# Kernel optimization log

Hardware: AMD Instinct MI355X
Metric: run time of the kernel (lower is better)

## Reference

```python
import jax, jax.numpy as jnp
import numpy as np

N_NODES = 50000
N_EDGES = 800000
D = 128
# PNA avg_deg['log'] from deg histogram: all 50000 nodes have degree 16
# avg_deg_log = sum(log(i+1)*deg[i]) / sum(deg) = log(17)
AVG_DEG_LOG = float(np.log(17.0))
EPS = 1e-5  # PyG StdAggregation epsilon


def setup_inputs() -> dict:
    key = jax.random.key(0)
    k1, k2, k3 = jax.random.split(key, 3)
    x = jax.random.normal(k1, (N_EDGES, D), jnp.float32)
    index = jax.random.randint(k2, (N_EDGES,), 0, N_NODES)
    # nn.Linear(12*D, D): weight [out, in]
    W = jax.random.normal(k3, (D, 12 * D), jnp.float32) * 0.02
    b = jnp.zeros((D,), jnp.float32)
    return {"x": x, "index": index, "W": W, "b": b}


def reference(x, index, W, b):
    N = N_NODES
    ones = jnp.ones((x.shape[0],), x.dtype)
    cnt = jax.ops.segment_sum(ones, index, num_segments=N)          # [N] degree
    cnt_c = jnp.maximum(cnt, 1.0)[:, None]                          # clamp(1)
    s1 = jax.ops.segment_sum(x, index, num_segments=N)              # [N, D]
    s2 = jax.ops.segment_sum(x * x, index, num_segments=N)          # [N, D]
    mean = s1 / cnt_c
    var = s2 / cnt_c - mean * mean
    std = jnp.sqrt(jax.nn.relu(var) + EPS)
    mn = jax.ops.segment_min(x, index, num_segments=N)
    mx = jax.ops.segment_max(x, index, num_segments=N)
    empty = (cnt == 0.0)[:, None]
    mn = jnp.where(empty, 0.0, mn)  # torch_scatter fills empty segments with 0
    mx = jnp.where(empty, 0.0, mx)
    agg = jnp.concatenate([mean, mn, mx, std], axis=-1)             # [N, 4D]
    logd = jnp.log(jnp.maximum(cnt, 1.0) + 1.0)[:, None]
    amp = agg * (logd / AVG_DEG_LOG)                                # amplification
    att = agg * (AVG_DEG_LOG / logd)                                # attenuation
    out = jnp.concatenate([agg, amp, att], axis=-1)                 # [N, 12D]
    return out @ W.T + b                                            # [N, D]
```

## Files before the change

kernel.cpp:

```cpp
#include <hip/hip_runtime.h>
#include <hip/hip_bf16.h>

typedef __attribute__((ext_vector_type(8))) __bf16 bf16x8;
typedef __attribute__((ext_vector_type(4))) float f32x4;

#define AVG_DEG_LOG 2.833213344056216f

__device__ __forceinline__ unsigned short f2bf(float f) {
  union { float f; unsigned int u; } a; a.f = f;
  unsigned int r = a.u + 0x7FFFu + ((a.u >> 16) & 1u);
  return (unsigned short)(r >> 16);
}

__device__ __forceinline__ uint2 pack4(f32x4 a) {
  uint2 u;
  u.x = (unsigned)f2bf(a[0]) | ((unsigned)f2bf(a[1]) << 16);
  u.y = (unsigned)f2bf(a[2]) | ((unsigned)f2bf(a[3]) << 16);
  return u;
}

__global__ void hist_wconv_kernel(const int* __restrict__ idx, int* __restrict__ cnt, int E,
                                  int hb, const float* __restrict__ W,
                                  unsigned short* __restrict__ Wb, int n4) {
  int b = blockIdx.x;
  if (b < hb) {
    int i = b * 256 + threadIdx.x;
    if (i < E) atomicAdd(&cnt[idx[i]], 1);
  } else {
    int i = (b - hb) * 256 + threadIdx.x;
    if (i < n4) {
      float4 v = ((const float4*)W)[i];
      ushort4 o;
      o.x = f2bf(v.x); o.y = f2bf(v.y); o.z = f2bf(v.z); o.w = f2bf(v.w);
      ((ushort4*)Wb)[i] = o;
    }
  }
}

__global__ __launch_bounds__(1024) void scan_kernel(const int* __restrict__ cnt,
                                                    int* __restrict__ offsets, int N) {
  __shared__ int partial[1024];
  int t = threadIdx.x;
  int CH = (N + 1023) >> 10;
  int base = t * CH;
  int s = 0;
  for (int i = 0; i < CH; ++i) { int id = base + i; if (id < N) s += cnt[id]; }
  partial[t] = s;
  __syncthreads();
  int val = s;
  for (int off = 1; off < 1024; off <<= 1) {
    int add = (t >= off) ? partial[t - off] : 0;
    __syncthreads();
    val += add;
    partial[t] = val;
    __syncthreads();
  }
  int run = val - s;
  for (int i = 0; i < CH; ++i) {
    int id = base + i;
    if (id < N) { offsets[id] = run; run += cnt[id]; }
  }
  if (t == 1023) offsets[N] = run;
}

__global__ void scatter_kernel(const int* __restrict__ idx, const int* __restrict__ offsets,
                               int* __restrict__ cursor, int* __restrict__ edge_ids, int E) {
  int i = blockIdx.x * blockDim.x + threadIdx.x;
  if (i < E) {
    int n = idx[i];
    int p = atomicAdd(&cursor[n], 1);
    edge_ids[offsets[n] + p] = i;
  }
}

__global__ __launch_bounds__(256) void agg_kernel(const float* __restrict__ x,
    const int* __restrict__ edge_ids, const int* __restrict__ offsets,
    unsigned short* __restrict__ agg4, float* __restrict__ amp, float* __restrict__ att, int Nn) {
  int wid = blockIdx.x * 4 + (threadIdx.x >> 6);
  if (wid >= Nn) return;
  int lane = threadIdx.x & 63;
  int half = lane >> 5;
  int fh = (lane & 31) * 4;
  int offs = offsets[wid];
  int deg = offsets[wid + 1] - offs;
  f32x4 s = {0.f, 0.f, 0.f, 0.f}, q = {0.f, 0.f, 0.f, 0.f};
  f32x4 mn = {INFINITY, INFINITY, INFINITY, INFINITY};
  f32x4 mx = {-INFINITY, -INFINITY, -INFINITY, -INFINITY};
  const float* xb = x + fh;
  for (int i = 0; i < deg; i += 64) {
    int myid = 0;
    if (i + lane < deg) myid = edge_ids[offs + i + lane];
    int c = deg - i; if (c > 64) c = 64;
    for (int ii = 0; ii < c; ii += 16) {
      int e[8];
      bool val[8];
#pragma unroll
      for (int k = 0; k < 8; ++k) {
        int p = ii + 2 * k + half;
        val[k] = p < c;
        int pc = val[k] ? p : c - 1;
        e[k] = __shfl(myid, pc, 64);
      }
      f32x4 v[8];
#pragma unroll
      for (int k = 0; k < 8; ++k)
        v[k] = __builtin_nontemporal_load((const f32x4*)(xb + (size_t)e[k] * 128));
#pragma unroll
      for (int k = 0; k < 8; ++k) {
#pragma unroll
        for (int j = 0; j < 4; ++j) {
          float f = v[k][j];
          float fs = val[k] ? f : 0.f;
          s[j] += fs;
          q[j] += f * fs;
          mn[j] = fminf(mn[j], val[k] ? f : INFINITY);
          mx[j] = fmaxf(mx[j], val[k] ? f : -INFINITY);
        }
      }
    }
  }
#pragma unroll
  for (int j = 0; j < 4; ++j) {
    s[j] += __shfl_xor(s[j], 32, 64);
    q[j] += __shfl_xor(q[j], 32, 64);
    mn[j] = fminf(mn[j], __shfl_xor(mn[j], 32, 64));
    mx[j] = fmaxf(mx[j], __shfl_xor(mx[j], 32, 64));
  }
  float cdeg = deg > 0 ? (float)deg : 1.0f;
  float inv = 1.0f / cdeg;
  f32x4 mean, sd;
#pragma unroll
  for (int j = 0; j < 4; ++j) {
    mean[j] = s[j] * inv;
    float var = q[j] * inv - mean[j] * mean[j];
    var = var > 0.f ? var : 0.f;
    sd[j] = sqrtf(var + 1e-5f);
  }
  if (deg == 0) {
#pragma unroll
    for (int j = 0; j < 4; ++j) { mn[j] = 0.f; mx[j] = 0.f; }
  }
  size_t rb = (size_t)wid * 512;
  if (half == 0) {
    *(uint2*)(agg4 + rb + fh)       = pack4(mean);
    *(uint2*)(agg4 + rb + 128 + fh) = pack4(mn);
  } else {
    *(uint2*)(agg4 + rb + 256 + fh) = pack4(mx);
    *(uint2*)(agg4 + rb + 384 + fh) = pack4(sd);
  }
  if (lane == 0) {
    float ld = logf(cdeg + 1.0f);
    amp[wid] = ld / AVG_DEG_LOG;
    att[wid] = AVG_DEG_LOG / ld;
  }
}

__global__ __launch_bounds__(256) void gemm_kernel(
    const unsigned short* __restrict__ agg4, const unsigned short* __restrict__ Wb,
    const float* __restrict__ amp, const float* __restrict__ att,
    const float* __restrict__ bias, float* __restrict__ out, int Nn) {
  __shared__ __align__(16) unsigned short As[64][40];
  __shared__ __align__(16) unsigned short Bs[3][128][40];
  __shared__ float ampS[64], attS[64];
  int t = threadIdx.x;
  int m0 = blockIdx.x * 64;
  if (t < 64) {
    int n = m0 + t; if (n > Nn - 1) n = Nn - 1;
    ampS[t] = amp[n]; attS[t] = att[n];
  }
  int wave = t >> 6, lane = t & 63;
  int arow = lane & 15, quad = lane >> 4;
  f32x4 acc[3][8];
#pragma unroll
  for (int g = 0; g < 3; ++g)
#pragma unroll
    for (int c8 = 0; c8 < 8; ++c8) acc[g][c8] = (f32x4){0.f, 0.f, 0.f, 0.f};

  int ar = t >> 2;
  int akc = (t & 3) * 8;
  int agr = m0 + ar; if (agr > Nn - 1) agr = Nn - 1;
  const unsigned short* aptr = agg4 + (size_t)agr * 512 + akc;

  for (int kk = 0; kk < 512; kk += 32) {
    __syncthreads();
    *(uint4*)&As[ar][akc] = *(const uint4*)(aptr + kk);
#pragma unroll
    for (int j = 0; j < 6; ++j) {
      int idx = t + j * 256;
      int g = idx >> 9;
      int rem = idx & 511;
      int n = rem >> 2;
      int kc = (rem & 3) * 8;
      *(uint4*)&Bs[g][n][kc] = *(const uint4*)(Wb + (size_t)n * 1536 + g * 512 + kk + kc);
    }
    __syncthreads();
    bf16x8 af = *(bf16x8*)&As[wave * 16 + arow][quad * 8];
#pragma unroll
    for (int g = 0; g < 3; ++g) {
#pragma unroll
      for (int c8 = 0; c8 < 8; ++c8) {
        bf16x8 bf = *(bf16x8*)&Bs[g][c8 * 16 + arow][quad * 8];
        acc[g][c8] = __builtin_amdgcn_mfma_f32_16x16x32_bf16(af, bf, acc[g][c8], 0, 0, 0);
      }
    }
  }
#pragma unroll
  for (int c8 = 0; c8 < 8; ++c8) {
    int col = c8 * 16 + arow;
    float bv = bias[col];
#pragma unroll
    for (int r = 0; r < 4; ++r) {
      int lrow = wave * 16 + quad * 4 + r;
      int n = m0 + lrow;
      if (n < Nn) {
        float o = acc[0][c8][r] + ampS[lrow] * acc[1][c8][r] + attS[lrow] * acc[2][c8][r] + bv;
        out[(size_t)n * 128 + col] = o;
      }
    }
  }
}

extern "C" void kernel_launch(void* const* d_in, const int* in_sizes, int n_in,
                              void* d_out, int out_size, void* d_ws, size_t ws_size,
                              hipStream_t stream) {
  const float* x     = (const float*)d_in[0];
  const int*   index = (const int*)d_in[1];
  const float* W     = (const float*)d_in[2];
  const float* bias  = (const float*)d_in[3];
  int E  = in_sizes[1];
  int Nn = out_size / 128;
  float* out = (float*)d_out;

  char* ws = (char*)d_ws;
  size_t off = 0;
  int* cnt     = (int*)(ws + off); off += (size_t)Nn * 4;
  int* cursor  = (int*)(ws + off); off += (size_t)Nn * 4;
  int* offsets = (int*)(ws + off); off += (size_t)(Nn + 1) * 4;
  off = (off + 255) & ~(size_t)255;
  int* edge_ids = (int*)(ws + off); off += (size_t)E * 4;
  off = (off + 255) & ~(size_t)255;
  unsigned short* agg4 = (unsigned short*)(ws + off); off += (size_t)Nn * 512 * 2;
  float* amp = (float*)(ws + off); off += (size_t)Nn * 4;
  float* att = (float*)(ws + off); off += (size_t)Nn * 4;
  off = (off + 255) & ~(size_t)255;
  unsigned short* Wb = (unsigned short*)(ws + off); off += (size_t)128 * 1536 * 2;

  hipMemsetAsync(ws, 0, (size_t)Nn * 8, stream);

  int eb = (E + 255) / 256;
  int n4 = 128 * 1536 / 4;
  int wb = (n4 + 255) / 256;
  hist_wconv_kernel<<<eb + wb, 256, 0, stream>>>(index, cnt, E, eb, W, Wb, n4);
  scan_kernel<<<1, 1024, 0, stream>>>(cnt, offsets, Nn);
  scatter_kernel<<<eb, 256, 0, stream>>>(index, offsets, cursor, edge_ids, E);
  agg_kernel<<<(Nn + 3) / 4, 256, 0, stream>>>(x, edge_ids, offsets, agg4, amp, att, Nn);
  gemm_kernel<<<(Nn + 63) / 64, 256, 0, stream>>>(agg4, Wb, amp, att, bias, out, Nn);
}
```

Baseline: 755.1 us.

## Parallelize offset scan across blocks and aggregate two nodes per wave

```diff
diff --git a/kernel.cpp b/kernel.cpp
--- a/kernel.cpp
+++ b/kernel.cpp
@@ -37,30 +37,57 @@
   }
 }
 
-__global__ __launch_bounds__(1024) void scan_kernel(const int* __restrict__ cnt,
-                                                    int* __restrict__ offsets, int N) {
-  __shared__ int partial[1024];
+__global__ __launch_bounds__(256) void scan1_kernel(const int* __restrict__ cnt,
+                                                    int* __restrict__ bsums, int N) {
+  __shared__ int red[256];
   int t = threadIdx.x;
-  int CH = (N + 1023) >> 10;
-  int base = t * CH;
-  int s = 0;
-  for (int i = 0; i < CH; ++i) { int id = base + i; if (id < N) s += cnt[id]; }
-  partial[t] = s;
+  int i = blockIdx.x * 256 + t;
+  int v = (i < N) ? cnt[i] : 0;
+  red[t] = v;
   __syncthreads();
-  int val = s;
-  for (int off = 1; off < 1024; off <<= 1) {
-    int add = (t >= off) ? partial[t - off] : 0;
+  for (int o = 128; o > 0; o >>= 1) {
+    if (t < o) red[t] += red[t + o];
+    __syncthreads();
+  }
+  if (t == 0) bsums[blockIdx.x] = red[0];
+}
+
+__global__ __launch_bounds__(256) void scan2_kernel(int* __restrict__ bsums, int nb) {
+  __shared__ int sS[256];
+  int t = threadIdx.x;
+  int v = (t < nb) ? bsums[t] : 0;
+  sS[t] = v;
+  __syncthreads();
+  int val = v;
+  for (int o = 1; o < 256; o <<= 1) {
+    int add = (t >= o) ? sS[t - o] : 0;
     __syncthreads();
     val += add;
-    partial[t] = val;
-    __syncthreads();
-  }
-  int run = val - s;
-  for (int i = 0; i < CH; ++i) {
-    int id = base + i;
-    if (id < N) { offsets[id] = run; run += cnt[id]; }
-  }
-  if (t == 1023) offsets[N] = run;
+    sS[t] = val;
+    __syncthreads();
+  }
+  if (t < nb) bsums[t] = val - v;
+}
+
+__global__ __launch_bounds__(256) void scan3_kernel(const int* __restrict__ cnt,
+                                                    const int* __restrict__ bsums,
+                                                    int* __restrict__ offsets, int N, int E) {
+  __shared__ int sS[256];
+  int t = threadIdx.x;
+  int i = blockIdx.x * 256 + t;
+  int v = (i < N) ? cnt[i] : 0;
+  sS[t] = v;
+  __syncthreads();
+  int val = v;
+  for (int o = 1; o < 256; o <<= 1) {
+    int add = (t >= o) ? sS[t - o] : 0;
+    __syncthreads();
+    val += add;
+    sS[t] = val;
+    __syncthreads();
+  }
+  if (i < N) offsets[i] = bsums[blockIdx.x] + val - v;
+  if (blockIdx.x == 0 && t == 0) offsets[N] = E;
 }
 
 __global__ void scatter_kernel(const int* __restrict__ idx, const int* __restrict__ offsets,
@@ -73,52 +100,49 @@
   }
 }
 
-__global__ __launch_bounds__(256) void agg_kernel(const float* __restrict__ x,
-    const int* __restrict__ edge_ids, const int* __restrict__ offsets,
-    unsigned short* __restrict__ agg4, float* __restrict__ amp, float* __restrict__ att, int Nn) {
-  int wid = blockIdx.x * 4 + (threadIdx.x >> 6);
-  if (wid >= Nn) return;
-  int lane = threadIdx.x & 63;
-  int half = lane >> 5;
-  int fh = (lane & 31) * 4;
-  int offs = offsets[wid];
-  int deg = offsets[wid + 1] - offs;
-  f32x4 s = {0.f, 0.f, 0.f, 0.f}, q = {0.f, 0.f, 0.f, 0.f};
-  f32x4 mn = {INFINITY, INFINITY, INFINITY, INFINITY};
-  f32x4 mx = {-INFINITY, -INFINITY, -INFINITY, -INFINITY};
-  const float* xb = x + fh;
+__device__ __forceinline__ void agg_accum_chunk(const float* __restrict__ xb, int eid,
+    int ii, int deg, int half, f32x4& s, f32x4& q, f32x4& mn, f32x4& mx) {
+  int e[8];
+  bool val[8];
+#pragma unroll
+  for (int k = 0; k < 8; ++k) {
+    int p = ii + 2 * k + half;
+    val[k] = p < deg;
+    int pc = val[k] ? p : deg - 1;
+    e[k] = __shfl(eid, pc, 64);
+  }
+  f32x4 v[8];
+#pragma unroll
+  for (int k = 0; k < 8; ++k)
+    v[k] = __builtin_nontemporal_load((const f32x4*)(xb + (size_t)e[k] * 128));
+#pragma unroll
+  for (int k = 0; k < 8; ++k) {
+#pragma unroll
+    for (int j = 0; j < 4; ++j) {
+      float f = v[k][j];
+      float fs = val[k] ? f : 0.f;
+      s[j] += fs;
+      q[j] += f * fs;
+      mn[j] = fminf(mn[j], val[k] ? f : INFINITY);
+      mx[j] = fmaxf(mx[j], val[k] ? f : -INFINITY);
+    }
+  }
+}
+
+__device__ void agg_one(const float* __restrict__ xb, const int* __restrict__ edge_ids,
+    int offs, int deg, int lane, int half, f32x4& s, f32x4& q, f32x4& mn, f32x4& mx) {
   for (int i = 0; i < deg; i += 64) {
     int myid = 0;
     if (i + lane < deg) myid = edge_ids[offs + i + lane];
     int c = deg - i; if (c > 64) c = 64;
-    for (int ii = 0; ii < c; ii += 16) {
-      int e[8];
-      bool val[8];
-#pragma unroll
-      for (int k = 0; k < 8; ++k) {
-        int p = ii + 2 * k + half;
-        val[k] = p < c;
-        int pc = val[k] ? p : c - 1;
-        e[k] = __shfl(myid, pc, 64);
-      }
-      f32x4 v[8];
-#pragma unroll
-      for (int k = 0; k < 8; ++k)
-        v[k] = __builtin_nontemporal_load((const f32x4*)(xb + (size_t)e[k] * 128));
-#pragma unroll
-      for (int k = 0; k < 8; ++k) {
-#pragma unroll
-        for (int j = 0; j < 4; ++j) {
-          float f = v[k][j];
-          float fs = val[k] ? f : 0.f;
-          s[j] += fs;
-          q[j] += f * fs;
-          mn[j] = fminf(mn[j], val[k] ? f : INFINITY);
-          mx[j] = fmaxf(mx[j], val[k] ? f : -INFINITY);
-        }
-      }
-    }
-  }
+    for (int ii = 0; ii < c; ii += 16)
+      agg_accum_chunk(xb, myid, ii, c, half, s, q, mn, mx);
+  }
+}
+
+__device__ void agg_finish(unsigned short* __restrict__ agg4, float* __restrict__ amp,
+    float* __restrict__ att, int wid, int deg, int lane, int half, int fh,
+    f32x4 s, f32x4 q, f32x4 mn, f32x4 mx) {
 #pragma unroll
   for (int j = 0; j < 4; ++j) {
     s[j] += __shfl_xor(s[j], 32, 64);
@@ -153,6 +177,100 @@
     amp[wid] = ld / AVG_DEG_LOG;
     att[wid] = AVG_DEG_LOG / ld;
   }
+}
+
+__global__ __launch_bounds__(256) void agg_kernel(const float* __restrict__ x,
+    const int* __restrict__ edge_ids, const int* __restrict__ offsets,
+    unsigned short* __restrict__ agg4, float* __restrict__ amp, float* __restrict__ att, int Nn) {
+  int gw = blockIdx.x * 4 + (threadIdx.x >> 6);
+  int nA = gw * 2, nB = nA + 1;
+  if (nA >= Nn) return;
+  bool hasB = nB < Nn;
+  int lane = threadIdx.x & 63;
+  int half = lane >> 5;
+  int fh = (lane & 31) * 4;
+  const float* xb = x + fh;
+
+  int o0 = offsets[nA];
+  int o1 = offsets[nA + 1];
+  int o2 = hasB ? offsets[nB + 1] : o1;
+  int offsA = o0, degA = o1 - o0;
+  int offsB = o1, degB = hasB ? (o2 - o1) : 0;
+
+  f32x4 sA = {0,0,0,0}, qA = {0,0,0,0};
+  f32x4 mnA = {INFINITY,INFINITY,INFINITY,INFINITY}, mxA = {-INFINITY,-INFINITY,-INFINITY,-INFINITY};
+  f32x4 sB = {0,0,0,0}, qB = {0,0,0,0};
+  f32x4 mnB = {INFINITY,INFINITY,INFINITY,INFINITY}, mxB = {-INFINITY,-INFINITY,-INFINITY,-INFINITY};
+
+  if (degA <= 64 && degB <= 64) {
+    int eidA = 0, eidB = 0;
+    if (lane < degA) eidA = edge_ids[offsA + lane];
+    if (lane < degB) eidB = edge_ids[offsB + lane];
+    int cm = degA > degB ? degA : degB;
+    for (int ii = 0; ii < cm; ii += 16) {
+      bool doA = ii < degA;
+      bool doB = ii < degB;
+      int eA[8], eB[8];
+      bool valA[8], valB[8];
+      f32x4 vA[8], vB[8];
+      if (doA) {
+#pragma unroll
+        for (int k = 0; k < 8; ++k) {
+          int p = ii + 2 * k + half;
+          valA[k] = p < degA;
+          int pc = valA[k] ? p : degA - 1;
+          eA[k] = __shfl(eidA, pc, 64);
+        }
+#pragma unroll
+        for (int k = 0; k < 8; ++k)
+          vA[k] = __builtin_nontemporal_load((const f32x4*)(xb + (size_t)eA[k] * 128));
+      }
+      if (doB) {
+#pragma unroll
+        for (int k = 0; k < 8; ++k) {
+          int p = ii + 2 * k + half;
+          valB[k] = p < degB;
+          int pc = valB[k] ? p : degB - 1;
+          eB[k] = __shfl(eidB, pc, 64);
+        }
+#pragma unroll
+        for (int k = 0; k < 8; ++k)
+          vB[k] = __builtin_nontemporal_load((const f32x4*)(xb + (size_t)eB[k] * 128));
+      }
+      if (doA) {
+#pragma unroll
+        for (int k = 0; k < 8; ++k) {
+#pragma unroll
+          for (int j = 0; j < 4; ++j) {
+            float f = vA[k][j];
+            float fs = valA[k] ? f : 0.f;
+            sA[j] += fs; qA[j] += f * fs;
+            mnA[j] = fminf(mnA[j], valA[k] ? f : INFINITY);
+            mxA[j] = fmaxf(mxA[j], valA[k] ? f : -INFINITY);
+          }
+        }
+      }
+      if (doB) {
+#pragma unroll
+        for (int k = 0; k < 8; ++k) {
+#pragma unroll
+          for (int j = 0; j < 4; ++j) {
+            float f = vB[k][j];
+            float fs = valB[k] ? f : 0.f;
+            sB[j] += fs; qB[j] += f * fs;
+            mnB[j] = fminf(mnB[j], valB[k] ? f : INFINITY);
+            mxB[j] = fmaxf(mxB[j], valB[k] ? f : -INFINITY);
+          }
+        }
+      }
+    }
+  } else {
+    agg_one(xb, edge_ids, offsA, degA, lane, half, sA, qA, mnA, mxA);
+    if (hasB) agg_one(xb, edge_ids, offsB, degB, lane, half, sB, qB, mnB, mxB);
+  }
+
+  agg_finish(agg4, amp, att, nA, degA, lane, half, fh, sA, qA, mnA, mxA);
+  if (hasB) agg_finish(agg4, amp, att, nB, degB, lane, half, fh, sB, qB, mnB, mxB);
 }
 
 __global__ __launch_bounds__(256) void gemm_kernel(
@@ -237,6 +355,8 @@
   int* cursor  = (int*)(ws + off); off += (size_t)Nn * 4;
   int* offsets = (int*)(ws + off); off += (size_t)(Nn + 1) * 4;
   off = (off + 255) & ~(size_t)255;
+  int* bsums   = (int*)(ws + off); off += (size_t)256 * 4;
+  off = (off + 255) & ~(size_t)255;
   int* edge_ids = (int*)(ws + off); off += (size_t)E * 4;
   off = (off + 255) & ~(size_t)255;
   unsigned short* agg4 = (unsigned short*)(ws + off); off += (size_t)Nn * 512 * 2;
@@ -250,9 +370,12 @@
   int eb = (E + 255) / 256;
   int n4 = 128 * 1536 / 4;
   int wb = (n4 + 255) / 256;
+  int nb = (Nn + 255) / 256;
   hist_wconv_kernel<<<eb + wb, 256, 0, stream>>>(index, cnt, E, eb, W, Wb, n4);
-  scan_kernel<<<1, 1024, 0, stream>>>(cnt, offsets, Nn);
+  scan1_kernel<<<nb, 256, 0, stream>>>(cnt, bsums, Nn);
+  scan2_kernel<<<1, 256, 0, stream>>>(bsums, nb);
+  scan3_kernel<<<nb, 256, 0, stream>>>(cnt, bsums, offsets, Nn, E);
   scatter_kernel<<<eb, 256, 0, stream>>>(index, offsets, cursor, edge_ids, E);
-  agg_kernel<<<(Nn + 3) / 4, 256, 0, stream>>>(x, edge_ids, offsets, agg4, amp, att, Nn);
+  agg_kernel<<<(Nn + 7) / 8, 256, 0, stream>>>(x, edge_ids, offsets, agg4, amp, att, Nn);
   gemm_kernel<<<(Nn + 63) / 64, 256, 0, stream>>>(agg4, Wb, amp, att, bias, out, Nn);
 }
```

New measurement: 692.3 us. 1.09x faster.
